# Optimization experiments

Measured on AMD Instinct MI355X. Metric: run time of the kernel, lower is better.

The kernel has to match this reference:

```python
import jax, jax.numpy as jnp
import numpy as np

# --- grid constants (from init_kwargs) ---
VOXEL = jnp.array([0.2, 0.2, 6.0], dtype=jnp.float32)
PC_MIN = jnp.array([-51.2, -51.2, -3.0], dtype=jnp.float32)
PC_MAX = jnp.array([51.2, 51.2, 3.0], dtype=jnp.float32)
NY, NX = 512, 512          # pseudo_image_dims
NSEG = NY * NX             # dense pillar grid used as segment space
BN_EPS = 1e-3


def setup_inputs() -> dict:
    key = jax.random.key(0)
    k1, k2 = jax.random.split(key)
    B, N, C = 2, 100000, 64
    # points roughly spanning the range, slightly beyond so some get filtered
    pts = jax.random.uniform(k1, (B, N, 3), dtype=jnp.float32)
    lo = jnp.array([-56.0, -56.0, -3.5], dtype=jnp.float32)
    hi = jnp.array([56.0, 56.0, 3.5], dtype=jnp.float32)
    points = lo + pts * (hi - lo)
    W = jax.random.normal(k2, (9, C), dtype=jnp.float32) * 0.1
    return {
        "points": points,
        "W": W,
        "gamma": jnp.ones((C,), jnp.float32),
        "beta": jnp.zeros((C,), jnp.float32),
        "running_mean": jnp.zeros((C,), jnp.float32),
        "running_var": jnp.ones((C,), jnp.float32),
    }


def _embed_one(pts, W, gamma, beta, r_mean, r_var):
    # pts: [N,3] -> pseudo-image [C, NY, NX]
    coords = jnp.floor((pts - PC_MIN) / VOXEL).astype(jnp.int32)        # [N,3] (x,y,z)
    in_range = jnp.all((pts >= PC_MIN) & (pts < PC_MAX), axis=-1)       # [N]
    pid = coords[:, 1] * NX + coords[:, 0]                              # pillar id = y*nx + x
    pid = jnp.where(in_range, pid, 0)
    w = in_range.astype(pts.dtype)[:, None]                             # [N,1] mask weight

    cnt = jax.ops.segment_sum(w[:, 0], pid, num_segments=NSEG)          # [NSEG]
    safe_cnt = jnp.maximum(cnt, 1.0)

    # cluster center offset: per-pillar mean of xyz
    sum_xyz = jax.ops.segment_sum(pts * w, pid, num_segments=NSEG)      # [NSEG,3]
    mean_xyz = sum_xyz / safe_cnt[:, None]
    f_cluster = pts - mean_xyz[pid]

    # voxel center offset
    center = (coords.astype(pts.dtype) + 0.5) * VOXEL + PC_MIN
    f_center = pts - center

    feats = jnp.concatenate([pts, f_cluster, f_center], axis=-1)        # [N,9]

    # PFN layer: Linear(9->C, no bias) + BN1d (eval, running stats) + ReLU
    h = feats @ W                                                       # [N,C]
    h = (h - r_mean) * jax.lax.rsqrt(r_var + BN_EPS) * gamma + beta
    h = jax.nn.relu(h)

    # scatter-avg per pillar, then dense canvas
    vsum = jax.ops.segment_sum(h * w, pid, num_segments=NSEG)           # [NSEG,C]
    vfeat = vsum / safe_cnt[:, None]
    return vfeat.reshape(NY, NX, -1).transpose(2, 0, 1)                 # [C,NY,NX]


def reference(points, W, gamma, beta, running_mean, running_var):
    # points: [B,N,3] -> pseudo-image [B,C,NY,NX]
    return jax.vmap(_embed_one, in_axes=(0, None, None, None, None, None))(
        points, W, gamma, beta, running_mean, running_var)
```

## Files before the change

kernel.cpp:

```cpp
#include <hip/hip_runtime.h>
#include <math.h>

#define NXg 512
#define NYg 512
#define NSEG (NXg * NYg)
#define CCH 64
#define CAP 16
#define SLOTS 4
#define PSTR 5
#define PPB 64
#define BN_EPS 1e-3f

#define PCMINX (-51.2f)
#define PCMINY (-51.2f)
#define PCMINZ (-3.0f)
#define PCMAXX (51.2f)
#define PCMAXY (51.2f)
#define PCMAXZ (3.0f)
#define VOXX (0.2f)
#define VOXY (0.2f)
#define VOXZ (6.0f)

#define RECIPX 5.0f
#define RECIPY 5.0f
#define RECIPZ (__uint_as_float(0x3E2AAAABu))

__device__ __forceinline__ int calc_pid(float x, float y, float z) {
    bool in_range = (x >= PCMINX) && (x < PCMAXX) &&
                    (y >= PCMINY) && (y < PCMAXY) &&
                    (z >= PCMINZ) && (z < PCMAXZ);
    if (!in_range) return -1;
    int cx = (int)floorf((x - PCMINX) * RECIPX);
    int cy = (int)floorf((y - PCMINY) * RECIPY);
    int p = cy * NXg + cx;
    return (p >= 0 && p < NSEG) ? p : -1;
}

__global__ void k1_bin(const float* __restrict__ pts, unsigned* __restrict__ cnt,
                       float4* __restrict__ bucket, int B, int N) {
    int i = blockIdx.x * blockDim.x + threadIdx.x;
    if (i >= B * N) return;
    const float* p = pts + (size_t)i * 3;
    float x = p[0], y = p[1], z = p[2];
    int pd = calc_pid(x, y, z);
    if (pd < 0) return;
    int b = i / N;
    int g = b * NSEG + pd;
    unsigned slot = atomicAdd(&cnt[g], 1u);
    if (slot < CAP) {
        float4 e; e.x = x; e.y = y; e.z = z; e.w = 0.0f;
        bucket[(size_t)g * CAP + slot] = e;
    }
}

__global__ void __launch_bounds__(256) k4_compute(
    const unsigned* __restrict__ cnt, const float4* __restrict__ bucket,
    const float* __restrict__ W, const float* __restrict__ gamma,
    const float* __restrict__ beta, const float* __restrict__ rmean,
    const float* __restrict__ rvar, float* __restrict__ out) {
    __shared__ float pxs[PPB * PSTR];
    __shared__ float pys[PPB * PSTR];
    __shared__ float pzs[PPB * PSTR];
    __shared__ float mxs[PPB], mys[PPB], mzs[PPB];
    __shared__ int ks[PPB];
    __shared__ float tile[CCH * 65];

    int t = threadIdx.x;
    int lane = t & 63;
    int wave = t >> 6;
    int gp0 = blockIdx.x * PPB;

    float w0 = W[0 * CCH + lane], w1 = W[1 * CCH + lane], w2 = W[2 * CCH + lane];
    float w3 = W[3 * CCH + lane], w4 = W[4 * CCH + lane], w5 = W[5 * CCH + lane];
    float w6 = W[6 * CCH + lane], w7 = W[7 * CCH + lane], w8 = W[8 * CCH + lane];
    float sc = gamma[lane] * (1.0f / sqrtf(rvar[lane] + BN_EPS));
    float shift = beta[lane] - rmean[lane] * sc;
    float Ac = (w0 + w3 + w6) * sc;
    float Bc = (w1 + w4 + w7) * sc;
    float Cc = (w2 + w5) * sc;
    float s3 = w3 * sc, s4 = w4 * sc, s5 = w5 * sc;
    float s6 = w6 * sc, s7 = w7 * sc, s8 = w8 * sc;

    {
        int p = t >> 2;
        int j = t & 3;
        int gp = gp0 + p;
        const float4* bk = bucket + (size_t)gp * CAP;
        float4 e = bk[j];
        unsigned kc = cnt[gp];
        int k = (kc < CAP) ? (int)kc : CAP;
        int kl = (k < SLOTS) ? k : SLOTS;
        bool valid = j < kl;
        float px = valid ? e.x : 0.f;
        float py = valid ? e.y : 0.f;
        float pz = valid ? e.z : 0.f;
        if (valid) {
            pxs[p * PSTR + j] = e.x;
            pys[p * PSTR + j] = e.y;
            pzs[p * PSTR + j] = e.z;
        }
        px += __shfl_xor(px, 1); py += __shfl_xor(py, 1); pz += __shfl_xor(pz, 1);
        px += __shfl_xor(px, 2); py += __shfl_xor(py, 2); pz += __shfl_xor(pz, 2);
        if (j == 0) {
            for (int jj = SLOTS; jj < k; ++jj) {
                float4 et = bk[jj];
                px += et.x; py += et.y; pz += et.z;
            }
            ks[p] = k;
            float fk = (k > 0) ? (float)k : 1.0f;
            mxs[p] = px / fk; mys[p] = py / fk; mzs[p] = pz / fk;
        }
    }
    __syncthreads();

    for (int it = 0; it < 16; ++it) {
        int ppl = wave * 16 + it;
        int k = ks[ppl];
        float acc = 0.0f;
        if (k > 0) {
            float mx = mxs[ppl], my = mys[ppl], mz = mzs[ppl];
            int pid = (gp0 + ppl) & (NSEG - 1);
            float ctx = ((float)(pid & (NXg - 1)) + 0.5f) * VOXX + PCMINX;
            float cty = ((float)(pid >> 9) + 0.5f) * VOXY + PCMINY;
            float D = shift;
            D = fmaf(-mx, s3, D); D = fmaf(-my, s4, D); D = fmaf(-mz, s5, D);
            D = fmaf(-ctx, s6, D); D = fmaf(-cty, s7, D);
            int kl = (k < SLOTS) ? k : SLOTS;
            for (int j = 0; j < kl; ++j) {
                float x = pxs[ppl * PSTR + j];
                float y = pys[ppl * PSTR + j];
                float z = pzs[ppl * PSTR + j];
                float cz = floorf((z - PCMINZ) * RECIPZ);
                float ctz = (cz + 0.5f) * VOXZ + PCMINZ;
                float h = fmaf(x, Ac, fmaf(y, Bc, fmaf(z, Cc, fmaf(z - ctz, s8, D))));
                acc += fmaxf(h, 0.0f);
            }
            for (int j = SLOTS; j < k; ++j) {
                float4 e = bucket[(size_t)(gp0 + ppl) * CAP + j];
                float cz = floorf((e.z - PCMINZ) * RECIPZ);
                float ctz = (cz + 0.5f) * VOXZ + PCMINZ;
                float h = fmaf(e.x, Ac, fmaf(e.y, Bc, fmaf(e.z, Cc,
                              fmaf(e.z - ctz, s8, D))));
                acc += fmaxf(h, 0.0f);
            }
            acc /= (float)k;
        }
        tile[lane * 65 + ppl] = acc;
    }
    __syncthreads();

    int b = gp0 >> 18;
    int pbatch = gp0 & (NSEG - 1);
    size_t obase = (size_t)b * CCH * NSEG + (size_t)pbatch;
    for (int jj = 0; jj < 4; ++jj) {
        int idx = jj * 256 + t;
        int c = idx >> 4;
        int q = idx & 15;
        float4 v;
        v.x = tile[c * 65 + q * 4 + 0];
        v.y = tile[c * 65 + q * 4 + 1];
        v.z = tile[c * 65 + q * 4 + 2];
        v.w = tile[c * 65 + q * 4 + 3];
        *reinterpret_cast<float4*>(out + obase + (size_t)c * NSEG + q * 4) = v;
    }
}

extern "C" void kernel_launch(void* const* d_in, const int* in_sizes, int n_in,
                              void* d_out, int out_size, void* d_ws, size_t ws_size,
                              hipStream_t stream) {
    const float* points = (const float*)d_in[0];
    const float* W      = (const float*)d_in[1];
    const float* gamma  = (const float*)d_in[2];
    const float* beta   = (const float*)d_in[3];
    const float* rmean  = (const float*)d_in[4];
    const float* rvar   = (const float*)d_in[5];
    float* out = (float*)d_out;

    int B = out_size / (CCH * NSEG);
    int N = in_sizes[0] / (3 * B);
    int BN = B * NSEG;
    int total_pts = B * N;

    unsigned* cnt  = (unsigned*)d_ws;
    float4* bucket = (float4*)(cnt + BN);

    hipMemsetAsync(cnt, 0, (size_t)BN * sizeof(unsigned), stream);

    int blk = 256;
    int grd_pts = (total_pts + blk - 1) / blk;
    k1_bin<<<grd_pts, blk, 0, stream>>>(points, cnt, bucket, B, N);
    k4_compute<<<BN / PPB, blk, 0, stream>>>(cnt, bucket, W, gamma, beta,
                                             rmean, rvar, out);
}
```

Before: 49.97 us.

## Split pillar buckets into dense first-point array and overflow array

Stores each pillar's first point in a contiguous per-pillar array and the rest in a separate overflow array. In the compute kernel, one thread per pillar reads the first point with a coalesced load and walks the overflow entries only when the pillar has more than one point. With about 200k points over 524k pillars, most pillars are empty or hold a single point, so this avoids fetching four strided 16-byte slots per pillar. The cost is a serial per-pillar loop over overflow entries handled by a single thread, which replaces the earlier four-lane shuffle reduction.

```diff
diff --git a/kernel.cpp b/kernel.cpp
--- a/kernel.cpp
+++ b/kernel.cpp
@@ -6,6 +6,7 @@
 #define NSEG (NXg * NYg)
 #define CCH 64
 #define CAP 16
+#define ECAP 15
 #define SLOTS 4
 #define PSTR 5
 #define PPB 64
@@ -37,7 +38,8 @@
 }
 
 __global__ void k1_bin(const float* __restrict__ pts, unsigned* __restrict__ cnt,
-                       float4* __restrict__ bucket, int B, int N) {
+                       float4* __restrict__ first, float4* __restrict__ ext,
+                       int B, int N) {
     int i = blockIdx.x * blockDim.x + threadIdx.x;
     if (i >= B * N) return;
     const float* p = pts + (size_t)i * 3;
@@ -47,14 +49,14 @@
     int b = i / N;
     int g = b * NSEG + pd;
     unsigned slot = atomicAdd(&cnt[g], 1u);
-    if (slot < CAP) {
-        float4 e; e.x = x; e.y = y; e.z = z; e.w = 0.0f;
-        bucket[(size_t)g * CAP + slot] = e;
-    }
+    float4 e; e.x = x; e.y = y; e.z = z; e.w = 0.0f;
+    if (slot == 0) first[g] = e;
+    else if (slot < CAP) ext[(size_t)g * ECAP + (slot - 1)] = e;
 }
 
 __global__ void __launch_bounds__(256) k4_compute(
-    const unsigned* __restrict__ cnt, const float4* __restrict__ bucket,
+    const unsigned* __restrict__ cnt, const float4* __restrict__ first,
+    const float4* __restrict__ ext,
     const float* __restrict__ W, const float* __restrict__ gamma,
     const float* __restrict__ beta, const float* __restrict__ rmean,
     const float* __restrict__ rvar, float* __restrict__ out) {
@@ -81,35 +83,31 @@
     float s3 = w3 * sc, s4 = w4 * sc, s5 = w5 * sc;
     float s6 = w6 * sc, s7 = w7 * sc, s8 = w8 * sc;
 
-    {
-        int p = t >> 2;
-        int j = t & 3;
-        int gp = gp0 + p;
-        const float4* bk = bucket + (size_t)gp * CAP;
-        float4 e = bk[j];
+    if (t < PPB) {
+        int gp = gp0 + t;
+        float4 f0 = first[gp];
         unsigned kc = cnt[gp];
         int k = (kc < CAP) ? (int)kc : CAP;
-        int kl = (k < SLOTS) ? k : SLOTS;
-        bool valid = j < kl;
-        float px = valid ? e.x : 0.f;
-        float py = valid ? e.y : 0.f;
-        float pz = valid ? e.z : 0.f;
-        if (valid) {
-            pxs[p * PSTR + j] = e.x;
-            pys[p * PSTR + j] = e.y;
-            pzs[p * PSTR + j] = e.z;
+        ks[t] = k;
+        float sx = 0.f, sy = 0.f, sz = 0.f;
+        if (k > 0) {
+            sx = f0.x; sy = f0.y; sz = f0.z;
+            pxs[t * PSTR + 0] = f0.x;
+            pys[t * PSTR + 0] = f0.y;
+            pzs[t * PSTR + 0] = f0.z;
+            const float4* ex = ext + (size_t)gp * ECAP;
+            for (int j = 1; j < k; ++j) {
+                float4 e = ex[j - 1];
+                if (j < SLOTS) {
+                    pxs[t * PSTR + j] = e.x;
+                    pys[t * PSTR + j] = e.y;
+                    pzs[t * PSTR + j] = e.z;
+                }
+                sx += e.x; sy += e.y; sz += e.z;
+            }
         }
-        px += __shfl_xor(px, 1); py += __shfl_xor(py, 1); pz += __shfl_xor(pz, 1);
-        px += __shfl_xor(px, 2); py += __shfl_xor(py, 2); pz += __shfl_xor(pz, 2);
-        if (j == 0) {
-            for (int jj = SLOTS; jj < k; ++jj) {
-                float4 et = bk[jj];
-                px += et.x; py += et.y; pz += et.z;
-            }
-            ks[p] = k;
-            float fk = (k > 0) ? (float)k : 1.0f;
-            mxs[p] = px / fk; mys[p] = py / fk; mzs[p] = pz / fk;
-        }
+        float fk = (k > 0) ? (float)k : 1.0f;
+        mxs[t] = sx / fk; mys[t] = sy / fk; mzs[t] = sz / fk;
     }
     __syncthreads();
 
@@ -136,7 +134,7 @@
                 acc += fmaxf(h, 0.0f);
             }
             for (int j = SLOTS; j < k; ++j) {
-                float4 e = bucket[(size_t)(gp0 + ppl) * CAP + j];
+                float4 e = ext[(size_t)(gp0 + ppl) * ECAP + (j - 1)];
                 float cz = floorf((e.z - PCMINZ) * RECIPZ);
                 float ctz = (cz + 0.5f) * VOXZ + PCMINZ;
                 float h = fmaf(e.x, Ac, fmaf(e.y, Bc, fmaf(e.z, Cc,
@@ -181,14 +179,15 @@
     int BN = B * NSEG;
     int total_pts = B * N;
 
-    unsigned* cnt  = (unsigned*)d_ws;
-    float4* bucket = (float4*)(cnt + BN);
+    unsigned* cnt = (unsigned*)d_ws;
+    float4* first = (float4*)(cnt + BN);
+    float4* ext   = first + BN;
 
     hipMemsetAsync(cnt, 0, (size_t)BN * sizeof(unsigned), stream);
 
     int blk = 256;
     int grd_pts = (total_pts + blk - 1) / blk;
-    k1_bin<<<grd_pts, blk, 0, stream>>>(points, cnt, bucket, B, N);
-    k4_compute<<<BN / PPB, blk, 0, stream>>>(cnt, bucket, W, gamma, beta,
+    k1_bin<<<grd_pts, blk, 0, stream>>>(points, cnt, first, ext, B, N);
+    k4_compute<<<BN / PPB, blk, 0, stream>>>(cnt, first, ext, W, gamma, beta,
                                              rmean, rvar, out);
 }
```

After: 47.89 us. -4.2%, faster.
